# Kernel optimization log

Measured on AMD Instinct MI355X. Metric: run time of the kernel, lower is better.

The kernel has to match this reference:

```python
import jax, jax.numpy as jnp
import numpy as np

# Grid / time-stepping constants derived from init_kwargs
NX = 2046          # interior points; padded grid is NX+2 = 2048
N = NX + 2
DX = 14.0 / (NX + 1)   # (Lx_max - Lx_min) / (nx + 1)
DY = 14.0 / (NX + 1)
T_TOTAL = 0.032
NT = 16
DT = T_TOTAL / NT      # 0.002
NSTEPS = NT - 1        # evolve() skips i == 0
C2 = 1.0
M = 1.0


def setup_inputs() -> dict:
    key = jax.random.key(0)
    k1, k2 = jax.random.split(key)
    u0 = jax.random.normal(k1, (N, N), dtype=jnp.float32)
    v0 = jax.random.normal(k2, (N, N), dtype=jnp.float32)
    return {"u0": u0, "v0": v0}


def _grad_Vq(u):
    # 5-point Laplacian on the interior; boundary of the Laplacian buffer is zero
    # (torch writes into torch.zeros_like(u)). sin term applies on the FULL grid.
    lap = (u[2:, 1:-1] + u[:-2, 1:-1] - 2.0 * u[1:-1, 1:-1]) / (DX * DX) \
        + (u[1:-1, 2:] + u[1:-1, :-2] - 2.0 * u[1:-1, 1:-1]) / (DY * DY)
    lap = jnp.pad(lap, 1)  # zeros on the ghost ring, matching the torch buffer
    return C2 * lap - M * jnp.sin(u)


def _apply_bc(u, v):
    # homogeneous Neumann for u, zero v on edges (corners of v untouched)
    u = u.at[0, 1:-1].set(u[1, 1:-1])
    u = u.at[-1, 1:-1].set(u[-2, 1:-1])
    u = u.at[:, 0].set(u[:, 1])
    u = u.at[:, -1].set(u[:, -2])
    v = v.at[0, 1:-1].set(0.0)
    v = v.at[-1, 1:-1].set(0.0)
    v = v.at[1:-1, 0].set(0.0)
    v = v.at[1:-1, -1].set(0.0)
    return u, v


def _rk4_step(u, v):
    k1_v = DT * _grad_Vq(u)
    k2_v = DT * _grad_Vq(u + 0.5 * DT * v)
    k3_v = DT * _grad_Vq(u + 0.5 * DT * (v + 0.5 * k1_v))
    k4_v = DT * _grad_Vq(u + DT * (v + k3_v))
    k1_u = DT * v
    k2_u = DT * (v + 0.5 * k1_v)
    k3_u = DT * (v + 0.5 * k2_v)
    k4_u = DT * (v + k3_v)
    un = u + (k1_u + 2.0 * k2_u + 2.0 * k3_u + k4_u) / 6.0
    vn = v + (k1_v + 2.0 * k2_v + 2.0 * k3_v + k4_v) / 6.0
    return _apply_bc(un, vn)


def reference(u0, v0):
    def body(carry, _):
        u, v = carry
        u, v = _rk4_step(u, v)
        return (u, v), None

    (u, v), _ = jax.lax.scan(body, (u0, v0), None, length=NSTEPS)
    return jnp.stack([u, v])  # [2, N, N]: final fields u, v
```

## Files before the change

### kernel.cpp

```cpp
#include <hip/hip_runtime.h>
#include <math.h>

#define N 2048
#define NN (N * N)
#define NSTEPS 15

constexpr double DXd = 14.0 / 2047.0;
constexpr float DX2f = (float)(DXd * DXd);
constexpr float RDX2f = (float)(1.0 / (double)DX2f);
constexpr float SIXTHf = (float)(1.0 / 6.0);
constexpr float DTf  = (float)(0.032 / 16.0);
constexpr float HDTf = (float)(0.5 * (0.032 / 16.0));

__global__ __launch_bounds__(256) void step_kernel(
    const float* __restrict__ u, const float* __restrict__ v,
    float* __restrict__ un, float* __restrict__ vn)
{
    __shared__ float uL[38][39];
    __shared__ float vL[38][39];
    __shared__ float a3L[36][39];
    __shared__ float k3L[34][39];

    const int tx = threadIdx.x, ty = threadIdx.y;
    const int i0 = blockIdx.y * 32, j0 = blockIdx.x * 32;

    for (int r = ty; r < 38; r += 8) {
        int gi = i0 - 3 + r;
        gi = min(max(gi, 0), N - 1);
        for (int c = tx; c < 38; c += 32) {
            int gj = j0 - 3 + c;
            gj = min(max(gj, 0), N - 1);
            size_t g = (size_t)gi * N + gj;
            uL[r][c] = u[g];
            vL[r][c] = v[g];
        }
    }
    __syncthreads();

    for (int r = ty; r < 36; r += 8) {
        int gi = i0 - 2 + r;
        bool ringi = (gi <= 0) | (gi >= N - 1);
        for (int c = tx; c < 36; c += 32) {
            int gj = j0 - 2 + c;
            float uc = uL[r + 1][c + 1];
            float lap = 0.0f;
            if (!(ringi | (gj <= 0) | (gj >= N - 1))) {
                lap = (uL[r + 2][c + 1] + uL[r][c + 1] - 2.0f * uc) * RDX2f
                    + (uL[r + 1][c + 2] + uL[r + 1][c] - 2.0f * uc) * RDX2f;
            }
            float k1 = DTf * (lap - __sinf(uc));
            a3L[r][c] = uc + HDTf * (vL[r + 1][c + 1] + 0.5f * k1);
        }
    }
    __syncthreads();

    for (int r = ty; r < 34; r += 8) {
        int gi = i0 - 1 + r;
        bool ringi = (gi <= 0) | (gi >= N - 1);
        for (int c = tx; c < 34; c += 32) {
            int gj = j0 - 1 + c;
            float ac = a3L[r + 1][c + 1];
            float lap = 0.0f;
            if (!(ringi | (gj <= 0) | (gj >= N - 1))) {
                lap = (a3L[r + 2][c + 1] + a3L[r][c + 1] - 2.0f * ac) * RDX2f
                    + (a3L[r + 1][c + 2] + a3L[r + 1][c] - 2.0f * ac) * RDX2f;
            }
            k3L[r][c] = DTf * (lap - __sinf(ac));
        }
    }
    __syncthreads();

    for (int oi = ty; oi < 32; oi += 8) {
        const int gi = i0 + oi;
        const int oj = tx;
        const int gj = j0 + oj;

        float uc  = uL[oi + 3][oj + 3];
        float vc  = vL[oi + 3][oj + 3];
        float k3c = k3L[oi + 1][oj + 1];

        float a2c = uc + HDTf * vc;
        float a4c = uc + DTf * (vc + k3c);

        bool ring = (gi == 0) | (gi == N - 1) | (gj == 0) | (gj == N - 1);
        float lap1 = 0.0f, lap2 = 0.0f, lap4 = 0.0f;
        if (!ring) {
            lap1 = (uL[oi + 4][oj + 3] + uL[oi + 2][oj + 3] - 2.0f * uc) * RDX2f
                 + (uL[oi + 3][oj + 4] + uL[oi + 3][oj + 2] - 2.0f * uc) * RDX2f;

            float a2n = uL[oi + 2][oj + 3] + HDTf * vL[oi + 2][oj + 3];
            float a2s = uL[oi + 4][oj + 3] + HDTf * vL[oi + 4][oj + 3];
            float a2w = uL[oi + 3][oj + 2] + HDTf * vL[oi + 3][oj + 2];
            float a2e = uL[oi + 3][oj + 4] + HDTf * vL[oi + 3][oj + 4];
            lap2 = (a2s + a2n - 2.0f * a2c) * RDX2f
                 + (a2e + a2w - 2.0f * a2c) * RDX2f;

            float a4n = uL[oi + 2][oj + 3] + DTf * (vL[oi + 2][oj + 3] + k3L[oi    ][oj + 1]);
            float a4s = uL[oi + 4][oj + 3] + DTf * (vL[oi + 4][oj + 3] + k3L[oi + 2][oj + 1]);
            float a4w = uL[oi + 3][oj + 2] + DTf * (vL[oi + 3][oj + 2] + k3L[oi + 1][oj    ]);
            float a4e = uL[oi + 3][oj + 4] + DTf * (vL[oi + 3][oj + 4] + k3L[oi + 1][oj + 2]);
            lap4 = (a4s + a4n - 2.0f * a4c) * RDX2f
                 + (a4e + a4w - 2.0f * a4c) * RDX2f;
        }
        float k1c = DTf * (lap1 - __sinf(uc));
        float k2c = DTf * (lap2 - __sinf(a2c));
        float k4c = DTf * (lap4 - __sinf(a4c));

        float k1u = DTf * vc;
        float k2u = DTf * (vc + 0.5f * k1c);
        float k3u = DTf * (vc + 0.5f * k2c);
        float k4u = DTf * (vc + k3c);

        float unv = uc + (k1u + 2.0f * k2u + 2.0f * k3u + k4u) * SIXTHf;
        float vnv = vc + (k1c + 2.0f * k2c + 2.0f * k3c + k4c) * SIXTHf;

        const size_t idx = (size_t)gi * N + gj;
        if (!ring) {
            un[idx] = unv;
            vn[idx] = vnv;
            if (gi == 1)     un[(size_t)0 * N + gj]       = unv;
            if (gi == N - 2) un[(size_t)(N - 1) * N + gj] = unv;
            if (gj == 1)     un[(size_t)gi * N + 0]       = unv;
            if (gj == N - 2) un[(size_t)gi * N + (N - 1)] = unv;
            if (gi == 1 && gj == 1)         un[0]                             = unv;
            if (gi == 1 && gj == N - 2)     un[N - 1]                         = unv;
            if (gi == N - 2 && gj == 1)     un[(size_t)(N - 1) * N]           = unv;
            if (gi == N - 2 && gj == N - 2) un[(size_t)(N - 1) * N + (N - 1)] = unv;
        } else {
            bool corner = ((gi == 0) | (gi == N - 1)) & ((gj == 0) | (gj == N - 1));
            vn[idx] = corner ? vnv : 0.0f;
        }
    }
}

extern "C" void kernel_launch(void* const* d_in, const int* in_sizes, int n_in,
                              void* d_out, int out_size, void* d_ws, size_t ws_size,
                              hipStream_t stream) {
    const float* u0 = (const float*)d_in[0];
    const float* v0 = (const float*)d_in[1];
    float* out_u = (float*)d_out;
    float* out_v = out_u + NN;

    float* ws = (float*)d_ws;
    float* wu = ws;
    float* wv = ws + (size_t)NN;

    dim3 blk(32, 8, 1);
    dim3 grd(N / 32, N / 32, 1);

    const float* us = u0;
    const float* vs = v0;
    for (int s = 0; s < NSTEPS; ++s) {
        float *ud, *vd;
        if ((s & 1) == 0) { ud = out_u; vd = out_v; }
        else             { ud = wu;    vd = wv;    }
        step_kernel<<<grd, blk, 0, stream>>>(us, vs, ud, vd);
        us = ud; vs = vd;
    }
}
```

Measured before the change: 643.8 us.

## Fuse two RK4 time steps per kernel via temporal blocking with wider halos

Adds a kernel that advances two RK4 steps per launch. It loads a 6-deep halo tile into shared memory, computes the intermediate u/v fields in LDS (boundary conditions included), then runs the second step. The Laplacians of the stage inputs are also rewritten using the linearity of the Laplacian (LU, LV, LK), so fewer full stages are needed per step. This halves global memory round-trips and launches (7 double-step launches plus 1 single-step launch), in exchange for redundant halo computation, more shared memory per block (about 37 KB) and lower occupancy.

```diff
diff --git a/kernel.cpp b/kernel.cpp
--- a/kernel.cpp
+++ b/kernel.cpp
@@ -3,7 +3,6 @@
 
 #define N 2048
 #define NN (N * N)
-#define NSTEPS 15
 
 constexpr double DXd = 14.0 / 2047.0;
 constexpr float DX2f = (float)(DXd * DXd);
@@ -11,6 +10,185 @@
 constexpr float SIXTHf = (float)(1.0 / 6.0);
 constexpr float DTf  = (float)(0.032 / 16.0);
 constexpr float HDTf = (float)(0.5 * (0.032 / 16.0));
+
+__global__ __launch_bounds__(256) void step2_kernel(
+    const float* __restrict__ u, const float* __restrict__ v,
+    float* __restrict__ un, float* __restrict__ vn)
+{
+    __shared__ float u0L[44][44];
+    __shared__ float v0L[42][42];
+    __shared__ float aL [42][42];
+    __shared__ float kL [40][40];
+    __shared__ float u1L[38][38];
+    __shared__ float v1L[38][38];
+
+    const int t = threadIdx.y * 32 + threadIdx.x;
+    const int i0 = blockIdx.y * 32, j0 = blockIdx.x * 32;
+
+    for (int s = t; s < 44 * 44; s += 256) {
+        int r = s / 44, c = s % 44;
+        int gi = min(max(i0 - 6 + r, 0), N - 1);
+        int gj = min(max(j0 - 6 + c, 0), N - 1);
+        u0L[r][c] = u[(size_t)gi * N + gj];
+    }
+    for (int s = t; s < 42 * 42; s += 256) {
+        int r = s / 42, c = s % 42;
+        int gi = min(max(i0 - 5 + r, 0), N - 1);
+        int gj = min(max(j0 - 5 + c, 0), N - 1);
+        v0L[r][c] = v[(size_t)gi * N + gj];
+    }
+    __syncthreads();
+
+    for (int s = t; s < 42 * 42; s += 256) {
+        int r = s / 42, c = s % 42;
+        int gi = i0 - 5 + r, gj = j0 - 5 + c;
+        float uc = u0L[r + 1][c + 1];
+        float lap = 0.0f;
+        if (!((gi <= 0) | (gi >= N - 1) | (gj <= 0) | (gj >= N - 1))) {
+            lap = (u0L[r][c + 1] + u0L[r + 2][c + 1] + u0L[r + 1][c] + u0L[r + 1][c + 2]
+                   - 4.0f * uc) * RDX2f;
+        }
+        float k1 = DTf * (lap - __sinf(uc));
+        aL[r][c] = uc + HDTf * (v0L[r][c] + 0.5f * k1);
+    }
+    __syncthreads();
+
+    for (int s = t; s < 40 * 40; s += 256) {
+        int r = s / 40, c = s % 40;
+        int gi = i0 - 4 + r, gj = j0 - 4 + c;
+        float ac = aL[r + 1][c + 1];
+        float lap = 0.0f;
+        if (!((gi <= 0) | (gi >= N - 1) | (gj <= 0) | (gj >= N - 1))) {
+            lap = (aL[r][c + 1] + aL[r + 2][c + 1] + aL[r + 1][c] + aL[r + 1][c + 2]
+                   - 4.0f * ac) * RDX2f;
+        }
+        kL[r][c] = DTf * (lap - __sinf(ac));
+    }
+    __syncthreads();
+
+    for (int s = t; s < 38 * 38; s += 256) {
+        int r = s / 38, c = s % 38;
+        int gi = i0 - 3 + r, gj = j0 - 3 + c;
+        float uc  = u0L[r + 3][c + 3];
+        float vc  = v0L[r + 2][c + 2];
+        float k3c = kL[r + 1][c + 1];
+        bool ring = (gi <= 0) | (gi >= N - 1) | (gj <= 0) | (gj >= N - 1);
+        float LU = 0.0f, LV = 0.0f, LK = 0.0f;
+        if (!ring) {
+            LU = (u0L[r + 2][c + 3] + u0L[r + 4][c + 3] + u0L[r + 3][c + 2] + u0L[r + 3][c + 4]
+                  - 4.0f * uc) * RDX2f;
+            LV = (v0L[r + 1][c + 2] + v0L[r + 3][c + 2] + v0L[r + 2][c + 1] + v0L[r + 2][c + 3]
+                  - 4.0f * vc) * RDX2f;
+            LK = (kL[r][c + 1] + kL[r + 2][c + 1] + kL[r + 1][c] + kL[r + 1][c + 2]
+                  - 4.0f * k3c) * RDX2f;
+        }
+        float k1c = DTf * (LU - __sinf(uc));
+        float a2c = uc + HDTf * vc;
+        float k2c = DTf * (LU + HDTf * LV - __sinf(a2c));
+        float a4c = uc + DTf * (vc + k3c);
+        float k4c = DTf * (LU + DTf * (LV + LK) - __sinf(a4c));
+
+        float k1u = DTf * vc;
+        float k2u = DTf * (vc + 0.5f * k1c);
+        float k3u = DTf * (vc + 0.5f * k2c);
+        float k4u = DTf * (vc + k3c);
+        float unv = uc + (k1u + 2.0f * k2u + 2.0f * k3u + k4u) * SIXTHf;
+        float vnv = vc + (k1c + 2.0f * k2c + 2.0f * k3c + k4c) * SIXTHf;
+
+        if (!ring) {
+            u1L[r][c] = unv;
+            v1L[r][c] = vnv;
+            if (gi == 1     && r > 0)  u1L[r - 1][c] = unv;
+            if (gi == N - 2 && r < 37) u1L[r + 1][c] = unv;
+            if (gj == 1     && c > 0)  u1L[r][c - 1] = unv;
+            if (gj == N - 2 && c < 37) u1L[r][c + 1] = unv;
+            if (gi == 1     && gj == 1)     u1L[r - 1][c - 1] = unv;
+            if (gi == 1     && gj == N - 2) u1L[r - 1][c + 1] = unv;
+            if (gi == N - 2 && gj == 1)     u1L[r + 1][c - 1] = unv;
+            if (gi == N - 2 && gj == N - 2) u1L[r + 1][c + 1] = unv;
+        } else {
+            bool ingrid = (gi >= 0) & (gi <= N - 1) & (gj >= 0) & (gj <= N - 1);
+            bool corner = ((gi == 0) | (gi == N - 1)) & ((gj == 0) | (gj == N - 1));
+            v1L[r][c] = corner ? vnv : 0.0f;
+            if (!ingrid) { u1L[r][c] = 0.0f; v1L[r][c] = 0.0f; }
+        }
+    }
+    __syncthreads();
+
+    for (int s = t; s < 36 * 36; s += 256) {
+        int r = s / 36, c = s % 36;
+        int gi = i0 - 2 + r, gj = j0 - 2 + c;
+        float uc = u1L[r + 1][c + 1];
+        float lap = 0.0f;
+        if (!((gi <= 0) | (gi >= N - 1) | (gj <= 0) | (gj >= N - 1))) {
+            lap = (u1L[r][c + 1] + u1L[r + 2][c + 1] + u1L[r + 1][c] + u1L[r + 1][c + 2]
+                   - 4.0f * uc) * RDX2f;
+        }
+        float k1 = DTf * (lap - __sinf(uc));
+        aL[r][c] = uc + HDTf * (v1L[r + 1][c + 1] + 0.5f * k1);
+    }
+    __syncthreads();
+
+    for (int s = t; s < 34 * 34; s += 256) {
+        int r = s / 34, c = s % 34;
+        int gi = i0 - 1 + r, gj = j0 - 1 + c;
+        float ac = aL[r + 1][c + 1];
+        float lap = 0.0f;
+        if (!((gi <= 0) | (gi >= N - 1) | (gj <= 0) | (gj >= N - 1))) {
+            lap = (aL[r][c + 1] + aL[r + 2][c + 1] + aL[r + 1][c] + aL[r + 1][c + 2]
+                   - 4.0f * ac) * RDX2f;
+        }
+        kL[r][c] = DTf * (lap - __sinf(ac));
+    }
+    __syncthreads();
+
+    for (int s = t; s < 32 * 32; s += 256) {
+        int oi = s >> 5, oj = s & 31;
+        int gi = i0 + oi, gj = j0 + oj;
+        float uc  = u1L[oi + 3][oj + 3];
+        float vc  = v1L[oi + 3][oj + 3];
+        float k3c = kL[oi + 1][oj + 1];
+        bool ring = (gi == 0) | (gi == N - 1) | (gj == 0) | (gj == N - 1);
+        float LU = 0.0f, LV = 0.0f, LK = 0.0f;
+        if (!ring) {
+            LU = (u1L[oi + 2][oj + 3] + u1L[oi + 4][oj + 3] + u1L[oi + 3][oj + 2] + u1L[oi + 3][oj + 4]
+                  - 4.0f * uc) * RDX2f;
+            LV = (v1L[oi + 2][oj + 3] + v1L[oi + 4][oj + 3] + v1L[oi + 3][oj + 2] + v1L[oi + 3][oj + 4]
+                  - 4.0f * vc) * RDX2f;
+            LK = (kL[oi][oj + 1] + kL[oi + 2][oj + 1] + kL[oi + 1][oj] + kL[oi + 1][oj + 2]
+                  - 4.0f * k3c) * RDX2f;
+        }
+        float k1c = DTf * (LU - __sinf(uc));
+        float a2c = uc + HDTf * vc;
+        float k2c = DTf * (LU + HDTf * LV - __sinf(a2c));
+        float a4c = uc + DTf * (vc + k3c);
+        float k4c = DTf * (LU + DTf * (LV + LK) - __sinf(a4c));
+
+        float k1u = DTf * vc;
+        float k2u = DTf * (vc + 0.5f * k1c);
+        float k3u = DTf * (vc + 0.5f * k2c);
+        float k4u = DTf * (vc + k3c);
+        float unv = uc + (k1u + 2.0f * k2u + 2.0f * k3u + k4u) * SIXTHf;
+        float vnv = vc + (k1c + 2.0f * k2c + 2.0f * k3c + k4c) * SIXTHf;
+
+        const size_t idx = (size_t)gi * N + gj;
+        if (!ring) {
+            un[idx] = unv;
+            vn[idx] = vnv;
+            if (gi == 1)     un[(size_t)0 * N + gj]       = unv;
+            if (gi == N - 2) un[(size_t)(N - 1) * N + gj] = unv;
+            if (gj == 1)     un[(size_t)gi * N + 0]       = unv;
+            if (gj == N - 2) un[(size_t)gi * N + (N - 1)] = unv;
+            if (gi == 1 && gj == 1)         un[0]                             = unv;
+            if (gi == 1 && gj == N - 2)     un[N - 1]                         = unv;
+            if (gi == N - 2 && gj == 1)     un[(size_t)(N - 1) * N]           = unv;
+            if (gi == N - 2 && gj == N - 2) un[(size_t)(N - 1) * N + (N - 1)] = unv;
+        } else {
+            bool corner = ((gi == 0) | (gi == N - 1)) & ((gj == 0) | (gj == N - 1));
+            vn[idx] = corner ? vnv : 0.0f;
+        }
+    }
+}
 
 __global__ __launch_bounds__(256) void step_kernel(
     const float* __restrict__ u, const float* __restrict__ v,
@@ -142,19 +320,20 @@
     float* out_v = out_u + NN;
 
     float* ws = (float*)d_ws;
-    float* wu = ws;
-    float* wv = ws + (size_t)NN;
+    float* au = ws;
+    float* av = ws + (size_t)NN;
+    float* bu = ws + 2 * (size_t)NN;
+    float* bv = ws + 3 * (size_t)NN;
 
     dim3 blk(32, 8, 1);
     dim3 grd(N / 32, N / 32, 1);
 
-    const float* us = u0;
-    const float* vs = v0;
-    for (int s = 0; s < NSTEPS; ++s) {
-        float *ud, *vd;
-        if ((s & 1) == 0) { ud = out_u; vd = out_v; }
-        else             { ud = wu;    vd = wv;    }
-        step_kernel<<<grd, blk, 0, stream>>>(us, vs, ud, vd);
-        us = ud; vs = vd;
-    }
+    step2_kernel<<<grd, blk, 0, stream>>>(u0, v0, au, av);
+    step2_kernel<<<grd, blk, 0, stream>>>(au, av, bu, bv);
+    step2_kernel<<<grd, blk, 0, stream>>>(bu, bv, au, av);
+    step2_kernel<<<grd, blk, 0, stream>>>(au, av, bu, bv);
+    step2_kernel<<<grd, blk, 0, stream>>>(bu, bv, au, av);
+    step2_kernel<<<grd, blk, 0, stream>>>(au, av, bu, bv);
+    step2_kernel<<<grd, blk, 0, stream>>>(bu, bv, au, av);
+    step_kernel <<<grd, blk, 0, stream>>>(au, av, out_u, out_v);
 }
```

Measured after the change: 564.1 us. 12.4% less time.
